# Performance work log

Measured on AMD Instinct MI355X. Metric: run time of the kernel, lower is better.

Reference implementation:

```python
import jax, jax.numpy as jnp
import numpy as np

B, S, H, L, NH, HD, V, FF, NC = 8, 512, 768, 12, 12, 64, 21128, 3072, 6
MAX_REL = 64
EPS = 1e-12


def rel_pos_table(seq_len, depth=HD, max_rel=MAX_REL):
    # NeZha functional (sinusoidal) relative-position embeddings, [S, S, depth]
    r = np.arange(seq_len)
    dist = np.clip(r[None, :] - r[:, None], -max_rel, max_rel) + max_rel
    vocab = 2 * max_rel + 1
    pos = np.arange(vocab)[:, None].astype(np.float32)
    i = np.arange(depth)[None, :]
    angle = pos / np.power(10000.0, (2 * (i // 2)) / float(depth))
    table = np.where(i % 2 == 0, np.sin(angle), np.cos(angle)).astype(np.float32)
    return jnp.asarray(table[dist])


def layer_norm(x, g, b):
    mu = jnp.mean(x, axis=-1, keepdims=True)
    var = jnp.mean(jnp.square(x - mu), axis=-1, keepdims=True)
    return (x - mu) * jax.lax.rsqrt(var + EPS) * g + b


def setup_inputs() -> dict:
    key = jax.random.key(0)
    ks = jax.random.split(key, 32)
    sd = 0.02
    d = {
        'input_ids': jax.random.randint(ks[0], (B, S), 0, V, dtype=jnp.int32),
        'attention_mask': jnp.ones((B, S), dtype=jnp.int32),
        'word_emb': sd * jax.random.normal(ks[1], (V, H), jnp.float32),
        'pos_emb': sd * jax.random.normal(ks[2], (S, H), jnp.float32),
        'type_emb': sd * jax.random.normal(ks[3], (2, H), jnp.float32),
        'ln_emb_g': jnp.ones((H,), jnp.float32),
        'ln_emb_b': jnp.zeros((H,), jnp.float32),
        'Wq': sd * jax.random.normal(ks[4], (L, H, H), jnp.float32),
        'bq': jnp.zeros((L, H), jnp.float32),
        'Wk': sd * jax.random.normal(ks[5], (L, H, H), jnp.float32),
        'bk': jnp.zeros((L, H), jnp.float32),
        'Wv': sd * jax.random.normal(ks[6], (L, H, H), jnp.float32),
        'bv': jnp.zeros((L, H), jnp.float32),
        'Wo': sd * jax.random.normal(ks[7], (L, H, H), jnp.float32),
        'bo': jnp.zeros((L, H), jnp.float32),
        'ln1_g': jnp.ones((L, H), jnp.float32),
        'ln1_b': jnp.zeros((L, H), jnp.float32),
        'W1': sd * jax.random.normal(ks[8], (L, H, FF), jnp.float32),
        'b1': jnp.zeros((L, FF), jnp.float32),
        'W2': sd * jax.random.normal(ks[9], (L, FF, H), jnp.float32),
        'b2': jnp.zeros((L, H), jnp.float32),
        'ln2_g': jnp.ones((L, H), jnp.float32),
        'ln2_b': jnp.zeros((L, H), jnp.float32),
        'pool_W': sd * jax.random.normal(ks[10], (H, H), jnp.float32),
        'pool_b': jnp.zeros((H,), jnp.float32),
        'cls_W': sd * jax.random.normal(ks[11], (2 * H, NC), jnp.float32),
        'cls_b': jnp.zeros((NC,), jnp.float32),
    }
    return d


def nezha_forward(input_ids, attention_mask, word_emb, pos_emb, type_emb,
                  ln_emb_g, ln_emb_b, Wq, bq, Wk, bk, Wv, bv, Wo, bo,
                  ln1_g, ln1_b, W1, b1, W2, b2, ln2_g, ln2_b,
                  pool_W, pool_b, cls_W, cls_b):
    seq = input_ids.shape[1]
    rel = rel_pos_table(seq)  # [S, S, HD], shared for keys and values
    mask_bias = (1.0 - attention_mask.astype(jnp.float32)) * -10000.0  # [B, S]

    x = word_emb[input_ids] + pos_emb[:seq][None, :, :] + type_emb[0][None, None, :]
    x = layer_norm(x, ln_emb_g, ln_emb_b)

    scale = 1.0 / jnp.sqrt(jnp.asarray(HD, jnp.float32))
    for l in range(L):
        q = (x @ Wq[l] + bq[l]).reshape(B, seq, NH, HD)
        k = (x @ Wk[l] + bk[l]).reshape(B, seq, NH, HD)
        v = (x @ Wv[l] + bv[l]).reshape(B, seq, NH, HD)
        # content scores + relative-position key scores
        scores = jnp.einsum('bihd,bjhd->bhij', q, k) + jnp.einsum('bihd,ijd->bhij', q, rel)
        scores = scores * scale + mask_bias[:, None, None, :]
        attn = jax.nn.softmax(scores, axis=-1)
        # content context + relative-position value context
        ctx = jnp.einsum('bhij,bjhd->bihd', attn, v) + jnp.einsum('bhij,ijd->bihd', attn, rel)
        ctx = ctx.reshape(B, seq, H)
        x = layer_norm(x + ctx @ Wo[l] + bo[l], ln1_g[l], ln1_b[l])
        h = jax.nn.gelu(x @ W1[l] + b1[l], approximate=False)
        x = layer_norm(x + h @ W2[l] + b2[l], ln2_g[l], ln2_b[l])

    pooled = jnp.tanh(x[:, 0] @ pool_W + pool_b)        # [B, H]
    seq_avg = jnp.mean(x, axis=1)                        # [B, H] (unmasked, as in torch.mean)
    concat = jnp.concatenate([seq_avg, pooled], axis=1)  # [B, 2H]
    return concat @ cls_W + cls_b                        # [B, 6]


def reference(input_ids, attention_mask, word_emb, pos_emb, type_emb,
              ln_emb_g, ln_emb_b, Wq, bq, Wk, bk, Wv, bv, Wo, bo,
              ln1_g, ln1_b, W1, b1, W2, b2, ln2_g, ln2_b,
              pool_W, pool_b, cls_W, cls_b):
    return nezha_forward(input_ids, attention_mask, word_emb, pos_emb, type_emb,
                         ln_emb_g, ln_emb_b, Wq, bq, Wk, bk, Wv, bv, Wo, bo,
                         ln1_g, ln1_b, W1, b1, W2, b2, ln2_g, ln2_b,
                         pool_W, pool_b, cls_W, cls_b)
```

## Files before the change

kernel.cpp:

```cpp
#include <hip/hip_runtime.h>
#include <hip/hip_bf16.h>
#include <math.h>

typedef __hip_bfloat16 bf;

#define B_ 8
#define S_ 512
#define H_ 768
#define L_ 12
#define NH_ 12
#define HD_ 64
#define FF_ 3072
#define NC_ 6
#define BS_ (B_ * S_)
#define BSH_ ((size_t)BS_ * H_)
#define KAUG_ 672
#define TAUG_ 160
#define TPAD_ 144

typedef __attribute__((ext_vector_type(8))) short s16x8;
typedef __attribute__((ext_vector_type(4))) float fx4;

__device__ __forceinline__ float LD(const void* p, size_t i, int isbf) {
    return isbf ? __bfloat162float(((const bf*)p)[i]) : ((const float*)p)[i];
}

__device__ __forceinline__ void gload16(const void* g, void* l) {
    __builtin_amdgcn_global_load_lds(
        (const __attribute__((address_space(1))) void*)g,
        (__attribute__((address_space(3))) void*)l, 16, 0, 0);
}

__device__ __forceinline__ s16x8 ldfrag64(const unsigned short* base, int row, int chunk) {
    return *(const s16x8*)((const char*)base + row * 128 + ((chunk ^ (row & 7)) << 4));
}
__device__ __forceinline__ s16x8 ldfrag32(const unsigned short* base, int row, int chunk) {
    return *(const s16x8*)((const char*)base + row * 64 + ((chunk ^ (row & 3)) << 4));
}

__device__ __forceinline__ float wred_sum(float v) {
#pragma unroll
    for (int o = 32; o; o >>= 1) v += __shfl_xor(v, o, 64);
    return v;
}
__device__ __forceinline__ float wred_max(float v) {
#pragma unroll
    for (int o = 32; o; o >>= 1) v = fmaxf(v, __shfl_xor(v, o, 64));
    return v;
}

__global__ void detect_kernel(const unsigned int* __restrict__ g, int* __restrict__ flag) {
    if (threadIdx.x == 0 && blockIdx.x == 0)
        *flag = (g[0] == 0x3F800000u) ? 0 : 1;
}

__global__ void build_table_kernel(float* __restrict__ tab) {
    int idx = blockIdx.x * 256 + threadIdx.x;
    if (idx >= 129 * 64) return;
    int p = idx >> 6, d = idx & 63;
    double angle = (double)p / pow(10000.0, (double)(2 * (d / 2)) / 64.0);
    tab[idx] = (float)((d & 1) ? cos(angle) : sin(angle));
}

__global__ void build_tabT_kernel(const float* __restrict__ tab,
                                  bf* __restrict__ th, bf* __restrict__ tl) {
    int idx = blockIdx.x * 256 + threadIdx.x;
    if (idx >= 64 * TAUG_) return;
    int d = idx / TAUG_, t = idx % TAUG_;
    float v = (t < 129) ? tab[t * 64 + d] : 0.0f;
    bf h = __float2bfloat16(v);
    th[idx] = h;
    tl[idx] = __float2bfloat16(v - __bfloat162float(h));
}

__global__ void build_tabS_kernel(const float* __restrict__ tab,
                                  bf* __restrict__ th, bf* __restrict__ tl) {
    int idx = blockIdx.x * 256 + threadIdx.x;
    if (idx >= TPAD_ * 64) return;
    int t = idx >> 6;
    float v = (t < 129) ? tab[idx] : 0.0f;
    bf h = __float2bfloat16(v);
    th[idx] = h;
    tl[idx] = __float2bfloat16(v - __bfloat162float(h));
}

__global__ __launch_bounds__(256) void embed_kernel(
    const int* __restrict__ ids, const void* __restrict__ we,
    const void* __restrict__ pe, const void* __restrict__ te,
    float* __restrict__ y, const int* __restrict__ fl) {
    int isbf = *fl;
    int t = blockIdx.x;
    int s = t & (S_ - 1);
    int id = ids[t];
    size_t base = (size_t)t * H_;
    for (int c = threadIdx.x; c < H_; c += 256) {
        y[base + c] = LD(we, (size_t)id * H_ + c, isbf) +
                      LD(pe, (size_t)s * H_ + c, isbf) +
                      LD(te, c, isbf);
    }
}

__global__ void maskbias_kernel(const int* __restrict__ mask, float* __restrict__ mb) {
    int t = blockIdx.x * 256 + threadIdx.x;
    if (t < BS_) mb[t] = (1.0f - (float)mask[t]) * -10000.0f;
}

__global__ __launch_bounds__(256) void ln_kernel(
    float* out, bf* ohi, bf* olo, const float* a, const float* resid,
    const void* __restrict__ g, const void* __restrict__ b, size_t goff,
    const int* __restrict__ fl) {
    __shared__ float part[256];
    int isbf = *fl;
    int tid = threadIdx.x;
    size_t base = (size_t)blockIdx.x * H_;
    float v0 = a[base + tid];
    float v1 = a[base + tid + 256];
    float v2 = a[base + tid + 512];
    if (resid) {
        v0 += resid[base + tid];
        v1 += resid[base + tid + 256];
        v2 += resid[base + tid + 512];
    }
    part[tid] = v0 + v1 + v2;
    __syncthreads();
    for (int off = 128; off > 0; off >>= 1) {
        if (tid < off) part[tid] += part[tid + off];
        __syncthreads();
    }
    float mu = part[0] * (1.0f / (float)H_);
    __syncthreads();
    float d0 = v0 - mu, d1 = v1 - mu, d2 = v2 - mu;
    part[tid] = d0 * d0 + d1 * d1 + d2 * d2;
    __syncthreads();
    for (int off = 128; off > 0; off >>= 1) {
        if (tid < off) part[tid] += part[tid + off];
        __syncthreads();
    }
    float var = part[0] * (1.0f / (float)H_);
    float rs = 1.0f / sqrtf(var + 1e-12f);
    float o0 = d0 * rs * LD(g, goff + tid, isbf)       + LD(b, goff + tid, isbf);
    float o1 = d1 * rs * LD(g, goff + tid + 256, isbf) + LD(b, goff + tid + 256, isbf);
    float o2 = d2 * rs * LD(g, goff + tid + 512, isbf) + LD(b, goff + tid + 512, isbf);
    out[base + tid]       = o0;
    out[base + tid + 256] = o1;
    out[base + tid + 512] = o2;
    if (ohi) {
        bf h0 = __float2bfloat16(o0), h1 = __float2bfloat16(o1), h2 = __float2bfloat16(o2);
        ohi[base + tid]       = h0;
        ohi[base + tid + 256] = h1;
        ohi[base + tid + 512] = h2;
        olo[base + tid]       = __float2bfloat16(o0 - __bfloat162float(h0));
        olo[base + tid + 256] = __float2bfloat16(o1 - __bfloat162float(h1));
        olo[base + tid + 512] = __float2bfloat16(o2 - __bfloat162float(h2));
    }
}

__global__ __launch_bounds__(256) void transpose_split_kernel(
    const void* __restrict__ W, size_t woff, bf* __restrict__ th, bf* __restrict__ tl,
    int K, int N, const int* __restrict__ fl) {
    __shared__ float s[32][33];
    const int isbf = *fl;
    const int tx = threadIdx.x & 31, ty = threadIdx.x >> 5;
    const int k0 = blockIdx.x * 32, n0 = blockIdx.y * 32;
#pragma unroll
    for (int i = 0; i < 4; ++i) {
        int k = k0 + ty + i * 8;
        s[ty + i * 8][tx] = LD(W, woff + (size_t)k * N + (n0 + tx), isbf);
    }
    __syncthreads();
#pragma unroll
    for (int i = 0; i < 4; ++i) {
        int n = n0 + ty + i * 8;
        float v = s[tx][ty + i * 8];
        bf h = __float2bfloat16(v);
        bf l = __float2bfloat16(v - __bfloat162float(h));
        th[(size_t)n * K + k0 + tx] = h;
        tl[(size_t)n * K + k0 + tx] = l;
    }
}

__global__ __launch_bounds__(256, 2) void mgemm_kernel(
    const bf* __restrict__ Ah, const bf* __restrict__ Al,
    const bf* __restrict__ Bh, const bf* __restrict__ Bl,
    const void* __restrict__ bias, size_t boff,
    float* __restrict__ C, bf* __restrict__ Chi, bf* __restrict__ Clo,
    int M, int N, int K, int act, int split_out, const int* __restrict__ fl) {
    (void)M;
    __shared__ __align__(16) unsigned short Ahs[128][32];
    __shared__ __align__(16) unsigned short Als[128][32];
    __shared__ __align__(16) unsigned short Bhs[128][32];
    __shared__ __align__(16) unsigned short Bls[128][32];
    const int tid  = threadIdx.x;
    const int lane = tid & 63;
    const int wid  = tid >> 6;
    const int wr   = wid >> 1, wc = wid & 1;
    const int m0 = blockIdx.y * 128, n0 = blockIdx.x * 128;
    const int srow = lane >> 2;
    const int scol = (lane & 3) * 8;

    const fx4 fzero = {0.f, 0.f, 0.f, 0.f};
    fx4 acc[4][4];
#pragma unroll
    for (int i = 0; i < 4; ++i)
#pragma unroll
        for (int j = 0; j < 4; ++j) acc[i][j] = fzero;

    for (int k0 = 0; k0 < K; k0 += 32) {
#pragma unroll
        for (int t = 0; t < 2; ++t) {
            const int r = wid * 32 + t * 16;
            const size_t ga = (size_t)(m0 + r + srow) * K + (k0 + scol);
            const size_t gb = (size_t)(n0 + r + srow) * K + (k0 + scol);
            gload16(Ah + ga, &Ahs[r][0]);
            gload16(Al + ga, &Als[r][0]);
            gload16(Bh + gb, &Bhs[r][0]);
            gload16(Bl + gb, &Bls[r][0]);
        }
        __syncthreads();

        const int fr = lane & 15;
        const int ko = (lane >> 4) * 8;
        s16x8 ah[4], al[4], bh[4], bl[4];
#pragma unroll
        for (int f = 0; f < 4; ++f) {
            ah[f] = *(const s16x8*)&Ahs[wr * 64 + f * 16 + fr][ko];
            al[f] = *(const s16x8*)&Als[wr * 64 + f * 16 + fr][ko];
            bh[f] = *(const s16x8*)&Bhs[wc * 64 + f * 16 + fr][ko];
            bl[f] = *(const s16x8*)&Bls[wc * 64 + f * 16 + fr][ko];
        }
#pragma unroll
        for (int im = 0; im < 4; ++im)
#pragma unroll
            for (int in = 0; in < 4; ++in) {
                acc[im][in] = __builtin_amdgcn_mfma_f32_16x16x32_bf16(ah[im], bh[in], acc[im][in], 0, 0, 0);
                acc[im][in] = __builtin_amdgcn_mfma_f32_16x16x32_bf16(ah[im], bl[in], acc[im][in], 0, 0, 0);
                acc[im][in] = __builtin_amdgcn_mfma_f32_16x16x32_bf16(al[im], bh[in], acc[im][in], 0, 0, 0);
            }
        __syncthreads();
    }

    const int isbf = *fl;
    const int cr0 = m0 + wr * 64 + (lane >> 4) * 4;
    const int cc0 = n0 + wc * 64 + (lane & 15);
#pragma unroll
    for (int in = 0; in < 4; ++in) {
        const int col = cc0 + in * 16;
        const float bv = LD(bias, boff + col, isbf);
#pragma unroll
        for (int im = 0; im < 4; ++im) {
#pragma unroll
            for (int r = 0; r < 4; ++r) {
                const int row = cr0 + im * 16 + r;
                float v = acc[im][in][r] + bv;
                if (act) v = 0.5f * v * (1.0f + erff(v * 0.70710678118654752f));
                if (split_out) {
                    bf h = __float2bfloat16(v);
                    bf l = __float2bfloat16(v - __bfloat162float(h));
                    Chi[(size_t)row * N + col] = h;
                    Clo[(size_t)row * N + col] = l;
                } else {
                    C[(size_t)row * N + col] = v;
                }
            }
        }
    }
}

__global__ __launch_bounds__(256) void qrel_kernel(
    const bf* __restrict__ qh, const bf* __restrict__ ql,
    const bf* __restrict__ tabSh, const bf* __restrict__ tabSl,
    float* __restrict__ qrel, int b0) {
    const int tid = threadIdx.x, lane = tid & 63, wv = tid >> 6;
    const int rbase = blockIdx.x * 128;
    const int h = blockIdx.y;
    const int t0 = blockIdx.z * 48;
    const int fr = lane & 15, ko = (lane >> 4) * 8;
    const fx4 fz = {0.f, 0.f, 0.f, 0.f};
    fx4 acc[2][3];
#pragma unroll
    for (int m = 0; m < 2; ++m)
#pragma unroll
        for (int n = 0; n < 3; ++n) acc[m][n] = fz;
#pragma unroll
    for (int ks = 0; ks < 2; ++ks) {
        s16x8 a_h[2], a_l[2], b_h[3], b_l[3];
#pragma unroll
        for (int m = 0; m < 2; ++m) {
            const int row = rbase + wv * 32 + m * 16 + fr;
            const size_t ga = ((size_t)(b0 * S_) + row) * H_ + h * 64 + ks * 32 + ko;
            a_h[m] = *(const s16x8*)(qh + ga);
            a_l[m] = *(const s16x8*)(ql + ga);
        }
#pragma unroll
        for (int n = 0; n < 3; ++n) {
            const int trow = t0 + n * 16 + fr;
            const size_t gb = (size_t)trow * 64 + ks * 32 + ko;
            b_h[n] = *(const s16x8*)(tabSh + gb);
            b_l[n] = *(const s16x8*)(tabSl + gb);
        }
#pragma unroll
        for (int m = 0; m < 2; ++m)
#pragma unroll
            for (int n = 0; n < 3; ++n) {
                acc[m][n] = __builtin_amdgcn_mfma_f32_16x16x32_bf16(a_h[m], b_h[n], acc[m][n], 0, 0, 0);
                acc[m][n] = __builtin_amdgcn_mfma_f32_16x16x32_bf16(a_h[m], b_l[n], acc[m][n], 0, 0, 0);
                acc[m][n] = __builtin_amdgcn_mfma_f32_16x16x32_bf16(a_l[m], b_h[n], acc[m][n], 0, 0, 0);
            }
    }
    const int rr = (lane >> 4) * 4, cc = lane & 15;
#pragma unroll
    for (int m = 0; m < 2; ++m)
#pragma unroll
        for (int n = 0; n < 3; ++n)
#pragma unroll
            for (int r = 0; r < 3 + 1; ++r) {
                const int row = rbase + wv * 32 + m * 16 + rr + r;
                const int t = t0 + n * 16 + cc;
                const int bb = row >> 9, ii = row & (S_ - 1);
                qrel[(((size_t)bb * NH_ + h) * S_ + ii) * TPAD_ + t] = acc[m][n][r];
            }
}

__global__ __launch_bounds__(256, 2) void qk_kernel(
    const bf* __restrict__ qh, const bf* __restrict__ ql,
    const bf* __restrict__ kh, const bf* __restrict__ kl,
    float* __restrict__ sc, int b0) {
    __shared__ __align__(16) unsigned short Qh[128][64];
    __shared__ __align__(16) unsigned short Ql_[128][64];
    __shared__ __align__(16) unsigned short Kh[128][64];
    __shared__ __align__(16) unsigned short Kl[128][64];
    const int tid = threadIdx.x, lane = tid & 63, wv = tid >> 6;
    const int j0 = blockIdx.x * 128, i0 = blockIdx.y * 128;
    const int h = blockIdx.z % NH_, bb = blockIdx.z / NH_;
    const int b = b0 + bb;
    const int srow = lane >> 3;
    const int schunk = (lane & 7) ^ (srow & 7);
#pragma unroll
    for (int t = 0; t < 4; ++t) {
        const int r = wv * 32 + t * 8;
        const size_t ga = (size_t)(b * S_ + i0 + r + srow) * H_ + h * 64 + schunk * 8;
        const size_t gb = (size_t)(b * S_ + j0 + r + srow) * H_ + h * 64 + schunk * 8;
        gload16(qh + ga, &Qh[r][0]);
        gload16(ql + ga, &Ql_[r][0]);
        gload16(kh + gb, &Kh[r][0]);
        gload16(kl + gb, &Kl[r][0]);
    }
    __syncthreads();
    const int fr = lane & 15, g = lane >> 4;
    const int wr = wv >> 1, wc = wv & 1;
    const fx4 fz = {0.f, 0.f, 0.f, 0.f};
    fx4 acc[4][4];
#pragma unroll
    for (int i = 0; i < 4; ++i)
#pragma unroll
        for (int j = 0; j < 4; ++j) acc[i][j] = fz;
#pragma unroll
    for (int ks = 0; ks < 2; ++ks) {
        s16x8 ah[4], al[4], bh[4], bl[4];
#pragma unroll
        for (int m = 0; m < 4; ++m) {
            const int row = wr * 64 + m * 16 + fr;
            ah[m] = ldfrag64(&Qh[0][0], row, ks * 4 + g);
            al[m] = ldfrag64(&Ql_[0][0], row, ks * 4 + g);
        }
#pragma unroll
        for (int n = 0; n < 4; ++n) {
            const int row = wc * 64 + n * 16 + fr;
            bh[n] = ldfrag64(&Kh[0][0], row, ks * 4 + g);
            bl[n] = ldfrag64(&Kl[0][0], row, ks * 4 + g);
        }
#pragma unroll
        for (int m = 0; m < 4; ++m)
#pragma unroll
            for (int n = 0; n < 4; ++n) {
                acc[m][n] = __builtin_amdgcn_mfma_f32_16x16x32_bf16(ah[m], bh[n], acc[m][n], 0, 0, 0);
                acc[m][n] = __builtin_amdgcn_mfma_f32_16x16x32_bf16(ah[m], bl[n], acc[m][n], 0, 0, 0);
                acc[m][n] = __builtin_amdgcn_mfma_f32_16x16x32_bf16(al[m], bh[n], acc[m][n], 0, 0, 0);
            }
    }
    const int rr = (lane >> 4) * 4, cc = lane & 15;
#pragma unroll
    for (int m = 0; m < 4; ++m)
#pragma unroll
        for (int n = 0; n < 4; ++n)
#pragma unroll
            for (int r = 0; r < 4; ++r) {
                const int ii = i0 + wr * 64 + m * 16 + rr + r;
                const int jj = j0 + wc * 64 + n * 16 + cc;
                sc[(((size_t)bb * NH_ + h) * S_ + ii) * S_ + jj] = acc[m][n][r];
            }
}

__global__ __launch_bounds__(256) void smrel_kernel(
    const float* __restrict__ scores, const float* __restrict__ qrel,
    const float* __restrict__ mb,
    bf* __restrict__ pah, bf* __restrict__ pal, int b0) {
    const int lane = threadIdx.x & 63;
    const int wv = threadIdx.x >> 6;
    const int i = blockIdx.x * 4 + wv;
    const int h = blockIdx.y, bb = blockIdx.z;
    const int b = b0 + bb;
    const size_t srow = ((size_t)bb * NH_ + h) * S_ + i;
    const size_t qbase = srow * TPAD_;
    const float mbias = mb[b * S_ + lane] * 0.0f + 0.0f; (void)mbias;

    float s[8];
    float lmax = -1e30f;
#pragma unroll
    for (int rep = 0; rep < 8; ++rep) {
        const int j = lane + rep * 64;
        int t = j - i; t = t < -64 ? -64 : (t > 64 ? 64 : t);
        float v = (scores[srow * S_ + j] + qrel[qbase + t + 64]) * 0.125f + mb[b * S_ + j];
        s[rep] = v;
        lmax = fmaxf(lmax, v);
    }
    const float mx = wred_max(lmax);
    float lsum = 0.0f;
#pragma unroll
    for (int rep = 0; rep < 8; ++rep) {
        s[rep] = expf(s[rep] - mx);
        lsum += s[rep];
    }
    const float inv = 1.0f / wred_sum(lsum);

    const size_t rowbase = srow * KAUG_;
#pragma unroll
    for (int e = 0; e < 3; ++e) {
        const int t = lane + e * 64;
        if (t < TAUG_) {
            pah[rowbase + 512 + t] = __float2bfloat16(0.0f);
            pal[rowbase + 512 + t] = __float2bfloat16(0.0f);
        }
    }
    float s_lo = 0.0f, s_hi = 0.0f;
#pragma unroll
    for (int rep = 0; rep < 8; ++rep) {
        const int j = lane + rep * 64;
        const float v = s[rep] * inv;
        bf hh = __float2bfloat16(v);
        pah[rowbase + j] = hh;
        pal[rowbase + j] = __float2bfloat16(v - __bfloat162float(hh));
        const int d = j - i;
        if (d <= -64) s_lo += s[rep];
        else if (d >= 64) s_hi += s[rep];
        else {
            pah[rowbase + 512 + d + 64] = hh;
            pal[rowbase + 512 + d + 64] = __float2bfloat16(v - __bfloat162float(hh));
        }
    }
    s_lo = wred_sum(s_lo);
    s_hi = wred_sum(s_hi);
    if (lane == 0) {
        float v0 = s_lo * inv;
        bf h0 = __float2bfloat16(v0);
        pah[rowbase + 512] = h0;
        pal[rowbase + 512] = __float2bfloat16(v0 - __bfloat162float(h0));
        float v1 = s_hi * inv;
        bf h1 = __float2bfloat16(v1);
        pah[rowbase + 512 + 128] = h1;
        pal[rowbase + 512 + 128] = __float2bfloat16(v1 - __bfloat162float(h1));
    }
}

__global__ __launch_bounds__(256) void vaug_kernel(
    const bf* __restrict__ vh, const bf* __restrict__ vl,
    const bf* __restrict__ tabTh, const bf* __restrict__ tabTl,
    bf* __restrict__ vah, bf* __restrict__ val_, int b0) {
    __shared__ unsigned short tile[64][71];
    const int h = blockIdx.x, pl = blockIdx.y, bb = blockIdx.z;
    const int b = b0 + bb;
    const bf* src  = pl ? vl : vh;
    bf*       dst  = pl ? val_ : vah;
    const bf* tsrc = pl ? tabTl : tabTh;
    const int tid = threadIdx.x;
    const size_t dbase = ((size_t)bb * NH_ + h) * 64;
    for (int j0 = 0; j0 < S_; j0 += 64) {
        for (int idx = tid; idx < 4096; idx += 256) {
            int jj = idx >> 6, d = idx & 63;
            tile[jj][d] = *(const unsigned short*)&src[(size_t)(b * S_ + j0 + jj) * H_ + h * 64 + d];
        }
        __syncthreads();
        for (int idx = tid; idx < 4096; idx += 256) {
            int d = idx >> 6, jj = idx & 63;
            *(unsigned short*)&dst[(dbase + d) * KAUG_ + j0 + jj] = tile[jj][d];
        }
        __syncthreads();
    }
    for (int idx = tid; idx < 64 * TAUG_; idx += 256) {
        int d = idx / TAUG_, t = idx % TAUG_;
        *(unsigned short*)&dst[(dbase + d) * KAUG_ + 512 + t] =
            *(const unsigned short*)&tsrc[idx];
    }
}

__global__ __launch_bounds__(256, 2) void pv_kernel(
    const bf* __restrict__ pah, const bf* __restrict__ pal,
    const bf* __restrict__ vah, const bf* __restrict__ val_,
    bf* __restrict__ ch, bf* __restrict__ cl, int b0) {
    __shared__ __align__(16) unsigned short Ah[128][32];
    __shared__ __align__(16) unsigned short Al[128][32];
    __shared__ __align__(16) unsigned short Bh[64][32];
    __shared__ __align__(16) unsigned short Bl[64][32];
    const int tid = threadIdx.x, lane = tid & 63, wv = tid >> 6;
    const int h = blockIdx.x, i0 = blockIdx.y * 128, bb = blockIdx.z;
    const int b = b0 + bb;
    const int srow = lane >> 2;
    const int schunk = (lane & 3) ^ (srow & 3);
    const fx4 fz = {0.f, 0.f, 0.f, 0.f};
    fx4 acc[2][4];
#pragma unroll
    for (int m = 0; m < 2; ++m)
#pragma unroll
        for (int n = 0; n < 4; ++n) acc[m][n] = fz;

    for (int k0 = 0; k0 < KAUG_; k0 += 32) {
#pragma unroll
        for (int t = 0; t < 2; ++t) {
            const int r = wv * 32 + t * 16;
            const size_t ga = (((size_t)bb * NH_ + h) * S_ + i0 + r + srow) * KAUG_ + k0 + schunk * 8;
            gload16(pah + ga, &Ah[r][0]);
            gload16(pal + ga, &Al[r][0]);
        }
        {
            const int r = wv * 16;
            const size_t gb = (((size_t)bb * NH_ + h) * 64 + r + srow) * KAUG_ + k0 + schunk * 8;
            gload16(vah + gb, &Bh[r][0]);
            gload16(val_ + gb, &Bl[r][0]);
        }
        __syncthreads();
        const int fr = lane & 15, g = lane >> 4;
        s16x8 a_h[2], a_l[2], b_h[4], b_l[4];
#pragma unroll
        for (int m = 0; m < 2; ++m) {
            const int row = wv * 32 + m * 16 + fr;
            a_h[m] = ldfrag32(&Ah[0][0], row, g);
            a_l[m] = ldfrag32(&Al[0][0], row, g);
        }
#pragma unroll
        for (int n = 0; n < 4; ++n) {
            const int row = n * 16 + fr;
            b_h[n] = ldfrag32(&Bh[0][0], row, g);
            b_l[n] = ldfrag32(&Bl[0][0], row, g);
        }
#pragma unroll
        for (int m = 0; m < 2; ++m)
#pragma unroll
            for (int n = 0; n < 4; ++n) {
                acc[m][n] = __builtin_amdgcn_mfma_f32_16x16x32_bf16(a_h[m], b_h[n], acc[m][n], 0, 0, 0);
                acc[m][n] = __builtin_amdgcn_mfma_f32_16x16x32_bf16(a_h[m], b_l[n], acc[m][n], 0, 0, 0);
                acc[m][n] = __builtin_amdgcn_mfma_f32_16x16x32_bf16(a_l[m], b_h[n], acc[m][n], 0, 0, 0);
            }
        __syncthreads();
    }
    const int rr = (lane >> 4) * 4, cc = lane & 15;
#pragma unroll
    for (int m = 0; m < 2; ++m)
#pragma unroll
        for (int n = 0; n < 4; ++n)
#pragma unroll
            for (int r = 0; r < 4; ++r) {
                const int row = i0 + wv * 32 + m * 16 + rr + r;
                const int d = n * 16 + cc;
                const float v = acc[m][n][r];
                bf hh = __float2bfloat16(v);
                const size_t o = (size_t)(b * S_ + row) * H_ + h * 64 + d;
                ch[o] = hh;
                cl[o] = __float2bfloat16(v - __bfloat162float(hh));
            }
}

__global__ __launch_bounds__(256) void pool_kernel(
    const float* __restrict__ x, const void* __restrict__ pW,
    const void* __restrict__ pb, float* __restrict__ pooled,
    const int* __restrict__ fl) {
    int isbf = *fl;
    int b = blockIdx.x;
    const float* xr = x + (size_t)b * S_ * H_;
    for (int n = threadIdx.x; n < H_; n += 256) {
        float acc = LD(pb, n, isbf);
        for (int kx = 0; kx < H_; ++kx)
            acc += xr[kx] * LD(pW, (size_t)kx * H_ + n, isbf);
        pooled[b * H_ + n] = tanhf(acc);
    }
}

__global__ __launch_bounds__(256) void seqavg_kernel(
    const float* __restrict__ x, float* __restrict__ sa) {
    int b = blockIdx.x;
    for (int c = threadIdx.x; c < H_; c += 256) {
        float s = 0.0f;
        for (int j = 0; j < S_; ++j) s += x[((size_t)b * S_ + j) * H_ + c];
        sa[b * H_ + c] = s * (1.0f / (float)S_);
    }
}

__global__ void head_kernel(const float* __restrict__ sa, const float* __restrict__ pooled,
                            const void* __restrict__ cW, const void* __restrict__ cb,
                            void* __restrict__ out, const int* __restrict__ fl) {
    int isbf = *fl;
    int t = threadIdx.x;
    if (t >= B_ * NC_) return;
    int b = t / NC_, c = t % NC_;
    float acc = LD(cb, c, isbf);
    for (int kx = 0; kx < H_; ++kx)
        acc += sa[b * H_ + kx] * LD(cW, (size_t)kx * NC_ + c, isbf);
    for (int kx = 0; kx < H_; ++kx)
        acc += pooled[b * H_ + kx] * LD(cW, (size_t)(H_ + kx) * NC_ + c, isbf);
    if (isbf) ((bf*)out)[t] = __float2bfloat16(acc);
    else      ((float*)out)[t] = acc;
}

extern "C" void kernel_launch(void* const* d_in, const int* in_sizes, int n_in,
                              void* d_out, int out_size, void* d_ws, size_t ws_size,
                              hipStream_t stream) {
    (void)in_sizes; (void)n_in; (void)out_size;
    const int* ids   = (const int*)d_in[0];
    const int* amask = (const int*)d_in[1];
    const void* we  = d_in[2];
    const void* pe  = d_in[3];
    const void* te  = d_in[4];
    const void* lng = d_in[5];
    const void* lnb = d_in[6];
    const void* Wq  = d_in[7];
    const void* bq  = d_in[8];
    const void* Wk  = d_in[9];
    const void* bk  = d_in[10];
    const void* Wv  = d_in[11];
    const void* bv  = d_in[12];
    const void* Wo  = d_in[13];
    const void* bo  = d_in[14];
    const void* l1g = d_in[15];
    const void* l1b = d_in[16];
    const void* W1  = d_in[17];
    const void* b1  = d_in[18];
    const void* W2  = d_in[19];
    const void* b2  = d_in[20];
    const void* l2g = d_in[21];
    const void* l2b = d_in[22];
    const void* pW  = d_in[23];
    const void* pb  = d_in[24];
    const void* cW  = d_in[25];
    const void* cb  = d_in[26];

    char* cur = (char*)d_ws;
    auto alloc = [&](size_t bytes) -> char* {
        char* p = cur;
        cur += (bytes + 255) & ~(size_t)255;
        return p;
    };
    float* x    = (float*)alloc(BSH_ * 4);
    float* r0   = (float*)alloc(BSH_ * 4);
    float* r1f  = (float*)alloc(BSH_ * 4);
    float* r2f  = (float*)alloc(BSH_ * 4);
    float* r3f  = (float*)alloc(BSH_ * 4);
    float* z    = (float*)alloc(BSH_ * 4);
    float* tab  = (float*)alloc(129 * 64 * 4);
    float* mb   = (float*)alloc(BS_ * 4);
    float* pool = (float*)alloc(B_ * H_ * 4);
    float* sa   = (float*)alloc(B_ * H_ * 4);
    bf* tabTh   = (bf*)alloc(64 * TAUG_ * 2);
    bf* tabTl   = (bf*)alloc(64 * TAUG_ * 2);
    bf* tabSh   = (bf*)alloc(TPAD_ * 64 * 2);
    bf* tabSl   = (bf*)alloc(TPAD_ * 64 * 2);
    int* flag   = (int*)alloc(256);

    const size_t fixed = (size_t)(cur - (char*)d_ws);
    auto regA_sz = [&](int CB) {
        size_t wt = (size_t)2 * H_ * FF_ * 2;
        size_t qr = (size_t)CB * NH_ * S_ * TPAD_ * 4;
        return (wt > qr ? wt : qr);
    };
    auto regB_sz = [&](int CB) {
        size_t xs = (size_t)4 * BSH_;
        size_t sc = (size_t)CB * NH_ * S_ * S_ * 4;
        return (xs > sc ? xs : sc);
    };
    auto need = [&](int CB) {
        return fixed + regA_sz(CB) + regB_sz(CB)
             + (size_t)CB * NH_ * S_ * KAUG_ * 2 * 2
             + (size_t)CB * NH_ * 64 * KAUG_ * 2 * 2
             + 4096;
    };
    int CB = 8;
    while (CB > 1 && need(CB) > ws_size) CB >>= 1;

    char* regA = alloc(regA_sz(CB));
    char* regB = alloc(regB_sz(CB));
    bf* pah  = (bf*)alloc((size_t)CB * NH_ * S_ * KAUG_ * 2 * 2);
    bf* pal  = pah + (size_t)CB * NH_ * S_ * KAUG_;
    bf* vah  = (bf*)alloc((size_t)CB * NH_ * 64 * KAUG_ * 2 * 2);
    bf* val_ = vah + (size_t)CB * NH_ * 64 * KAUG_;

    bf*    wth   = (bf*)regA;
    bf*    wtl   = wth + (size_t)H_ * FF_;
    float* qrelb = (float*)regA;
    bf*    xh    = (bf*)regB;
    bf*    xl    = xh + BSH_;
    float* scb   = (float*)regB;

    bf* qh  = (bf*)r1f; bf* qlp = qh  + BSH_;
    bf* khp = (bf*)r2f; bf* klp = khp + BSH_;
    bf* vhp = (bf*)r3f; bf* vlp = vhp + BSH_;
    bf* ch  = (bf*)r0;  bf* cl  = ch  + BSH_;
    bf* hbh = (bf*)r0;
    bf* hbl = (bf*)r2f;

    detect_kernel<<<1, 64, 0, stream>>>((const unsigned int*)lng, flag);
    build_table_kernel<<<(129 * 64 + 255) / 256, 256, 0, stream>>>(tab);
    build_tabT_kernel<<<(64 * TAUG_ + 255) / 256, 256, 0, stream>>>(tab, tabTh, tabTl);
    build_tabS_kernel<<<(TPAD_ * 64 + 255) / 256, 256, 0, stream>>>(tab, tabSh, tabSl);
    maskbias_kernel<<<(BS_ + 255) / 256, 256, 0, stream>>>(amask, mb);
    embed_kernel<<<BS_, 256, 0, stream>>>(ids, we, pe, te, r0, flag);
    ln_kernel<<<BS_, 256, 0, stream>>>(x, xh, xl, r0, nullptr, lng, lnb, 0, flag);

    dim3 tpHH(H_ / 32, H_ / 32);
    dim3 tpHF(H_ / 32, FF_ / 32);
    dim3 tpFH(FF_ / 32, H_ / 32);
    dim3 gH(H_ / 128, BS_ / 128);
    dim3 gF(FF_ / 128, BS_ / 128);
    dim3 gQR(CB * S_ / 128, NH_, 3);
    dim3 gVA(NH_, 2, CB);
    dim3 gQK(4, 4, NH_ * CB);
    dim3 gSM(S_ / 4, NH_, CB);
    dim3 gPV(NH_, 4, CB);

    for (int l = 0; l < L_; ++l) {
        const size_t oHH = (size_t)l * H_ * H_;
        const size_t oH  = (size_t)l * H_;
        const size_t oHF = (size_t)l * H_ * FF_;
        const size_t oF  = (size_t)l * FF_;

        transpose_split_kernel<<<tpHH, 256, 0, stream>>>(Wq, oHH, wth, wtl, H_, H_, flag);
        mgemm_kernel<<<gH, 256, 0, stream>>>(xh, xl, wth, wtl, bq, oH,
                                             nullptr, qh, qlp, BS_, H_, H_, 0, 1, flag);
        transpose_split_kernel<<<tpHH, 256, 0, stream>>>(Wk, oHH, wth, wtl, H_, H_, flag);
        mgemm_kernel<<<gH, 256, 0, stream>>>(xh, xl, wth, wtl, bk, oH,
                                             nullptr, khp, klp, BS_, H_, H_, 0, 1, flag);
        transpose_split_kernel<<<tpHH, 256, 0, stream>>>(Wv, oHH, wth, wtl, H_, H_, flag);
        mgemm_kernel<<<gH, 256, 0, stream>>>(xh, xl, wth, wtl, bv, oH,
                                             nullptr, vhp, vlp, BS_, H_, H_, 0, 1, flag);

        for (int b0 = 0; b0 < B_; b0 += CB) {
            qrel_kernel<<<gQR, 256, 0, stream>>>(qh, qlp, tabSh, tabSl, qrelb, b0);
            vaug_kernel<<<gVA, 256, 0, stream>>>(vhp, vlp, tabTh, tabTl, vah, val_, b0);
            qk_kernel<<<gQK, 256, 0, stream>>>(qh, qlp, khp, klp, scb, b0);
            smrel_kernel<<<gSM, 256, 0, stream>>>(scb, qrelb, mb, pah, pal, b0);
            pv_kernel<<<gPV, 256, 0, stream>>>(pah, pal, vah, val_, ch, cl, b0);
        }

        transpose_split_kernel<<<tpHH, 256, 0, stream>>>(Wo, oHH, wth, wtl, H_, H_, flag);
        mgemm_kernel<<<gH, 256, 0, stream>>>(ch, cl, wth, wtl, bo, oH,
                                             r1f, nullptr, nullptr, BS_, H_, H_, 0, 0, flag);
        ln_kernel<<<BS_, 256, 0, stream>>>(x, xh, xl, r1f, x, l1g, l1b, oH, flag);

        transpose_split_kernel<<<tpHF, 256, 0, stream>>>(W1, oHF, wth, wtl, H_, FF_, flag);
        mgemm_kernel<<<gF, 256, 0, stream>>>(xh, xl, wth, wtl, b1, oF,
                                             nullptr, hbh, hbl, BS_, FF_, H_, 1, 1, flag);
        transpose_split_kernel<<<tpFH, 256, 0, stream>>>(W2, oHF, wth, wtl, FF_, H_, flag);
        mgemm_kernel<<<gH, 256, 0, stream>>>(hbh, hbl, wth, wtl, b2, oH,
                                             z, nullptr, nullptr, BS_, H_, FF_, 0, 0, flag);
        ln_kernel<<<BS_, 256, 0, stream>>>(x, xh, xl, z, x, l2g, l2b, oH, flag);
    }

    pool_kernel<<<B_, 256, 0, stream>>>(x, pW, pb, pool, flag);
    seqavg_kernel<<<B_, 256, 0, stream>>>(x, sa);
    head_kernel<<<1, 64, 0, stream>>>(sa, pool, cW, cb, d_out, flag);
}
```

Baseline: 7.814 ms.

## Fuse QKV projections into one GEMM, add 64-row GEMM tiles, warp-per-row layernorm

Transposes Wq/Wk/Wv into one concatenated weight buffer, precomputes a concatenated fp32 bias, and runs a single GEMM with row stride 2304 so attention kernels read Q/K/V through a stride argument. The GEMM is templated on row tiles, and the H-output GEMMs use 64-row tiles to double block count for the small-N cases. Layernorm now uses one wavefront per row with shuffle reductions instead of a 256-thread block with shared-memory tree reductions. These aim to cut launch count, improve occupancy on narrow GEMMs, and remove barrier-heavy reductions, at the cost of a larger QKV buffer and workspace layout changes.

```diff
diff --git a/kernel.cpp b/kernel.cpp
--- a/kernel.cpp
+++ b/kernel.cpp
@@ -17,6 +17,7 @@
 #define KAUG_ 672
 #define TAUG_ 160
 #define TPAD_ 144
+#define QSTR_ 2304
 
 typedef __attribute__((ext_vector_type(8))) short s16x8;
 typedef __attribute__((ext_vector_type(4))) float fx4;
@@ -50,8 +51,10 @@
 }
 
 __global__ void detect_kernel(const unsigned int* __restrict__ g, int* __restrict__ flag) {
-    if (threadIdx.x == 0 && blockIdx.x == 0)
-        *flag = (g[0] == 0x3F800000u) ? 0 : 1;
+    if (threadIdx.x == 0 && blockIdx.x == 0) {
+        flag[0] = (g[0] == 0x3F800000u) ? 0 : 1;
+        flag[1] = 0;
+    }
 }
 
 __global__ void build_table_kernel(float* __restrict__ tab) {
@@ -105,53 +108,49 @@
     if (t < BS_) mb[t] = (1.0f - (float)mask[t]) * -10000.0f;
 }
 
+__global__ void biascat_kernel(const void* __restrict__ bq, const void* __restrict__ bk,
+                               const void* __restrict__ bv, size_t off,
+                               float* __restrict__ out, const int* __restrict__ fl) {
+    int isbf = *fl;
+    int t = blockIdx.x * 256 + threadIdx.x;
+    if (t >= 3 * H_) return;
+    const void* src = t < H_ ? bq : (t < 2 * H_ ? bk : bv);
+    out[t] = LD(src, off + (t % H_), isbf);
+}
+
 __global__ __launch_bounds__(256) void ln_kernel(
     float* out, bf* ohi, bf* olo, const float* a, const float* resid,
     const void* __restrict__ g, const void* __restrict__ b, size_t goff,
     const int* __restrict__ fl) {
-    __shared__ float part[256];
-    int isbf = *fl;
-    int tid = threadIdx.x;
-    size_t base = (size_t)blockIdx.x * H_;
-    float v0 = a[base + tid];
-    float v1 = a[base + tid + 256];
-    float v2 = a[base + tid + 512];
-    if (resid) {
-        v0 += resid[base + tid];
-        v1 += resid[base + tid + 256];
-        v2 += resid[base + tid + 512];
-    }
-    part[tid] = v0 + v1 + v2;
-    __syncthreads();
-    for (int off = 128; off > 0; off >>= 1) {
-        if (tid < off) part[tid] += part[tid + off];
-        __syncthreads();
-    }
-    float mu = part[0] * (1.0f / (float)H_);
-    __syncthreads();
-    float d0 = v0 - mu, d1 = v1 - mu, d2 = v2 - mu;
-    part[tid] = d0 * d0 + d1 * d1 + d2 * d2;
-    __syncthreads();
-    for (int off = 128; off > 0; off >>= 1) {
-        if (tid < off) part[tid] += part[tid + off];
-        __syncthreads();
-    }
-    float var = part[0] * (1.0f / (float)H_);
-    float rs = 1.0f / sqrtf(var + 1e-12f);
-    float o0 = d0 * rs * LD(g, goff + tid, isbf)       + LD(b, goff + tid, isbf);
-    float o1 = d1 * rs * LD(g, goff + tid + 256, isbf) + LD(b, goff + tid + 256, isbf);
-    float o2 = d2 * rs * LD(g, goff + tid + 512, isbf) + LD(b, goff + tid + 512, isbf);
-    out[base + tid]       = o0;
-    out[base + tid + 256] = o1;
-    out[base + tid + 512] = o2;
-    if (ohi) {
-        bf h0 = __float2bfloat16(o0), h1 = __float2bfloat16(o1), h2 = __float2bfloat16(o2);
-        ohi[base + tid]       = h0;
-        ohi[base + tid + 256] = h1;
-        ohi[base + tid + 512] = h2;
-        olo[base + tid]       = __float2bfloat16(o0 - __bfloat162float(h0));
-        olo[base + tid + 256] = __float2bfloat16(o1 - __bfloat162float(h1));
-        olo[base + tid + 512] = __float2bfloat16(o2 - __bfloat162float(h2));
+    const int isbf = *fl;
+    const int lane = threadIdx.x & 63, wv = threadIdx.x >> 6;
+    const int row = blockIdx.x * 4 + wv;
+    const size_t base = (size_t)row * H_;
+    float v[12];
+#pragma unroll
+    for (int e = 0; e < 12; ++e) {
+        const int c = lane + e * 64;
+        v[e] = a[base + c];
+        if (resid) v[e] += resid[base + c];
+    }
+    float s = 0.0f;
+#pragma unroll
+    for (int e = 0; e < 12; ++e) s += v[e];
+    const float mu = wred_sum(s) * (1.0f / (float)H_);
+    float q = 0.0f;
+#pragma unroll
+    for (int e = 0; e < 12; ++e) { v[e] -= mu; q += v[e] * v[e]; }
+    const float rs = 1.0f / sqrtf(wred_sum(q) * (1.0f / (float)H_) + 1e-12f);
+#pragma unroll
+    for (int e = 0; e < 12; ++e) {
+        const int c = lane + e * 64;
+        float o = v[e] * rs * LD(g, goff + c, isbf) + LD(b, goff + c, isbf);
+        out[base + c] = o;
+        if (ohi) {
+            bf h = __float2bfloat16(o);
+            ohi[base + c] = h;
+            olo[base + c] = __float2bfloat16(o - __bfloat162float(h));
+        }
     }
 }
 
@@ -179,40 +178,44 @@
     }
 }
 
+template<int MR>
 __global__ __launch_bounds__(256, 2) void mgemm_kernel(
     const bf* __restrict__ Ah, const bf* __restrict__ Al,
     const bf* __restrict__ Bh, const bf* __restrict__ Bl,
     const void* __restrict__ bias, size_t boff,
     float* __restrict__ C, bf* __restrict__ Chi, bf* __restrict__ Clo,
-    int M, int N, int K, int act, int split_out, const int* __restrict__ fl) {
-    (void)M;
-    __shared__ __align__(16) unsigned short Ahs[128][32];
-    __shared__ __align__(16) unsigned short Als[128][32];
+    int N, int K, int act, int split_out, const int* __restrict__ fl) {
+    __shared__ __align__(16) unsigned short Ahs[MR * 32][32];
+    __shared__ __align__(16) unsigned short Als[MR * 32][32];
     __shared__ __align__(16) unsigned short Bhs[128][32];
     __shared__ __align__(16) unsigned short Bls[128][32];
     const int tid  = threadIdx.x;
     const int lane = tid & 63;
     const int wid  = tid >> 6;
     const int wr   = wid >> 1, wc = wid & 1;
-    const int m0 = blockIdx.y * 128, n0 = blockIdx.x * 128;
+    const int m0 = blockIdx.y * (MR * 32), n0 = blockIdx.x * 128;
     const int srow = lane >> 2;
     const int scol = (lane & 3) * 8;
 
     const fx4 fzero = {0.f, 0.f, 0.f, 0.f};
-    fx4 acc[4][4];
-#pragma unroll
-    for (int i = 0; i < 4; ++i)
+    fx4 acc[MR][4];
+#pragma unroll
+    for (int i = 0; i < MR; ++i)
 #pragma unroll
         for (int j = 0; j < 4; ++j) acc[i][j] = fzero;
 
     for (int k0 = 0; k0 < K; k0 += 32) {
+#pragma unroll
+        for (int t = 0; t < MR / 2; ++t) {
+            const int r = wid * (MR * 8) + t * 16;
+            const size_t ga = (size_t)(m0 + r + srow) * K + (k0 + scol);
+            gload16(Ah + ga, &Ahs[r][0]);
+            gload16(Al + ga, &Als[r][0]);
+        }
 #pragma unroll
         for (int t = 0; t < 2; ++t) {
             const int r = wid * 32 + t * 16;
-            const size_t ga = (size_t)(m0 + r + srow) * K + (k0 + scol);
             const size_t gb = (size_t)(n0 + r + srow) * K + (k0 + scol);
-            gload16(Ah + ga, &Ahs[r][0]);
-            gload16(Al + ga, &Als[r][0]);
             gload16(Bh + gb, &Bhs[r][0]);
             gload16(Bl + gb, &Bls[r][0]);
         }
@@ -220,16 +223,19 @@
 
         const int fr = lane & 15;
         const int ko = (lane >> 4) * 8;
-        s16x8 ah[4], al[4], bh[4], bl[4];
+        s16x8 ah[MR], al[MR], bh[4], bl[4];
+#pragma unroll
+        for (int f = 0; f < MR; ++f) {
+            ah[f] = *(const s16x8*)&Ahs[wr * (MR * 16) + f * 16 + fr][ko];
+            al[f] = *(const s16x8*)&Als[wr * (MR * 16) + f * 16 + fr][ko];
+        }
 #pragma unroll
         for (int f = 0; f < 4; ++f) {
-            ah[f] = *(const s16x8*)&Ahs[wr * 64 + f * 16 + fr][ko];
-            al[f] = *(const s16x8*)&Als[wr * 64 + f * 16 + fr][ko];
             bh[f] = *(const s16x8*)&Bhs[wc * 64 + f * 16 + fr][ko];
             bl[f] = *(const s16x8*)&Bls[wc * 64 + f * 16 + fr][ko];
         }
 #pragma unroll
-        for (int im = 0; im < 4; ++im)
+        for (int im = 0; im < MR; ++im)
 #pragma unroll
             for (int in = 0; in < 4; ++in) {
                 acc[im][in] = __builtin_amdgcn_mfma_f32_16x16x32_bf16(ah[im], bh[in], acc[im][in], 0, 0, 0);
@@ -240,14 +246,14 @@
     }
 
     const int isbf = *fl;
-    const int cr0 = m0 + wr * 64 + (lane >> 4) * 4;
+    const int cr0 = m0 + wr * (MR * 16) + (lane >> 4) * 4;
     const int cc0 = n0 + wc * 64 + (lane & 15);
 #pragma unroll
     for (int in = 0; in < 4; ++in) {
         const int col = cc0 + in * 16;
         const float bv = LD(bias, boff + col, isbf);
 #pragma unroll
-        for (int im = 0; im < 4; ++im) {
+        for (int im = 0; im < MR; ++im) {
 #pragma unroll
             for (int r = 0; r < 4; ++r) {
                 const int row = cr0 + im * 16 + r;
@@ -269,7 +275,7 @@
 __global__ __launch_bounds__(256) void qrel_kernel(
     const bf* __restrict__ qh, const bf* __restrict__ ql,
     const bf* __restrict__ tabSh, const bf* __restrict__ tabSl,
-    float* __restrict__ qrel, int b0) {
+    float* __restrict__ qrel, int astr, int b0) {
     const int tid = threadIdx.x, lane = tid & 63, wv = tid >> 6;
     const int rbase = blockIdx.x * 128;
     const int h = blockIdx.y;
@@ -287,7 +293,7 @@
 #pragma unroll
         for (int m = 0; m < 2; ++m) {
             const int row = rbase + wv * 32 + m * 16 + fr;
-            const size_t ga = ((size_t)(b0 * S_) + row) * H_ + h * 64 + ks * 32 + ko;
+            const size_t ga = ((size_t)(b0 * S_) + row) * astr + h * 64 + ks * 32 + ko;
             a_h[m] = *(const s16x8*)(qh + ga);
             a_l[m] = *(const s16x8*)(ql + ga);
         }
@@ -313,7 +319,7 @@
 #pragma unroll
         for (int n = 0; n < 3; ++n)
 #pragma unroll
-            for (int r = 0; r < 3 + 1; ++r) {
+            for (int r = 0; r < 4; ++r) {
                 const int row = rbase + wv * 32 + m * 16 + rr + r;
                 const int t = t0 + n * 16 + cc;
                 const int bb = row >> 9, ii = row & (S_ - 1);
@@ -324,7 +330,7 @@
 __global__ __launch_bounds__(256, 2) void qk_kernel(
     const bf* __restrict__ qh, const bf* __restrict__ ql,
     const bf* __restrict__ kh, const bf* __restrict__ kl,
-    float* __restrict__ sc, int b0) {
+    float* __restrict__ sc, int astr, int b0) {
     __shared__ __align__(16) unsigned short Qh[128][64];
     __shared__ __align__(16) unsigned short Ql_[128][64];
     __shared__ __align__(16) unsigned short Kh[128][64];
@@ -338,8 +344,8 @@
 #pragma unroll
     for (int t = 0; t < 4; ++t) {
         const int r = wv * 32 + t * 8;
-        const size_t ga = (size_t)(b * S_ + i0 + r + srow) * H_ + h * 64 + schunk * 8;
-        const size_t gb = (size_t)(b * S_ + j0 + r + srow) * H_ + h * 64 + schunk * 8;
+        const size_t ga = (size_t)(b * S_ + i0 + r + srow) * astr + h * 64 + schunk * 8;
+        const size_t gb = (size_t)(b * S_ + j0 + r + srow) * astr + h * 64 + schunk * 8;
         gload16(qh + ga, &Qh[r][0]);
         gload16(ql + ga, &Ql_[r][0]);
         gload16(kh + gb, &Kh[r][0]);
@@ -402,7 +408,6 @@
     const int b = b0 + bb;
     const size_t srow = ((size_t)bb * NH_ + h) * S_ + i;
     const size_t qbase = srow * TPAD_;
-    const float mbias = mb[b * S_ + lane] * 0.0f + 0.0f; (void)mbias;
 
     float s[8];
     float lmax = -1e30f;
@@ -465,7 +470,7 @@
 __global__ __launch_bounds__(256) void vaug_kernel(
     const bf* __restrict__ vh, const bf* __restrict__ vl,
     const bf* __restrict__ tabTh, const bf* __restrict__ tabTl,
-    bf* __restrict__ vah, bf* __restrict__ val_, int b0) {
+    bf* __restrict__ vah, bf* __restrict__ val_, int astr, int b0) {
     __shared__ unsigned short tile[64][71];
     const int h = blockIdx.x, pl = blockIdx.y, bb = blockIdx.z;
     const int b = b0 + bb;
@@ -477,7 +482,7 @@
     for (int j0 = 0; j0 < S_; j0 += 64) {
         for (int idx = tid; idx < 4096; idx += 256) {
             int jj = idx >> 6, d = idx & 63;
-            tile[jj][d] = *(const unsigned short*)&src[(size_t)(b * S_ + j0 + jj) * H_ + h * 64 + d];
+            tile[jj][d] = *(const unsigned short*)&src[(size_t)(b * S_ + j0 + jj) * astr + h * 64 + d];
         }
         __syncthreads();
         for (int idx = tid; idx < 4096; idx += 256) {
@@ -658,11 +663,13 @@
     float* mb   = (float*)alloc(BS_ * 4);
     float* pool = (float*)alloc(B_ * H_ * 4);
     float* sa   = (float*)alloc(B_ * H_ * 4);
+    float* bqkv = (float*)alloc(3 * H_ * 4);
     bf* tabTh   = (bf*)alloc(64 * TAUG_ * 2);
     bf* tabTl   = (bf*)alloc(64 * TAUG_ * 2);
     bf* tabSh   = (bf*)alloc(TPAD_ * 64 * 2);
     bf* tabSl   = (bf*)alloc(TPAD_ * 64 * 2);
     int* flag   = (int*)alloc(256);
+    int* zflag  = flag + 1;
 
     const size_t fixed = (size_t)(cur - (char*)d_ws);
     auto regA_sz = [&](int CB) {
@@ -698,12 +705,11 @@
     bf*    xl    = xh + BSH_;
     float* scb   = (float*)regB;
 
-    bf* qh  = (bf*)r1f; bf* qlp = qh  + BSH_;
-    bf* khp = (bf*)r2f; bf* klp = khp + BSH_;
-    bf* vhp = (bf*)r3f; bf* vlp = vhp + BSH_;
-    bf* ch  = (bf*)r0;  bf* cl  = ch  + BSH_;
-    bf* hbh = (bf*)r0;
-    bf* hbl = (bf*)r2f;
+    bf* qkvh = (bf*)r1f;
+    bf* qkvl = qkvh + (size_t)BS_ * QSTR_;
+    bf* ch   = (bf*)r0;  bf* cl = ch + BSH_;
+    bf* hbh  = (bf*)r0;
+    bf* hbl  = (bf*)r2f;
 
     detect_kernel<<<1, 64, 0, stream>>>((const unsigned int*)lng, flag);
     build_table_kernel<<<(129 * 64 + 255) / 256, 256, 0, stream>>>(tab);
@@ -711,12 +717,13 @@
     build_tabS_kernel<<<(TPAD_ * 64 + 255) / 256, 256, 0, stream>>>(tab, tabSh, tabSl);
     maskbias_kernel<<<(BS_ + 255) / 256, 256, 0, stream>>>(amask, mb);
     embed_kernel<<<BS_, 256, 0, stream>>>(ids, we, pe, te, r0, flag);
-    ln_kernel<<<BS_, 256, 0, stream>>>(x, xh, xl, r0, nullptr, lng, lnb, 0, flag);
+    ln_kernel<<<BS_ / 4, 256, 0, stream>>>(x, xh, xl, r0, nullptr, lng, lnb, 0, flag);
 
     dim3 tpHH(H_ / 32, H_ / 32);
     dim3 tpHF(H_ / 32, FF_ / 32);
     dim3 tpFH(FF_ / 32, H_ / 32);
-    dim3 gH(H_ / 128, BS_ / 128);
+    dim3 gQKV(3 * H_ / 128, BS_ / 128);
+    dim3 gH64(H_ / 128, BS_ / 64);
     dim3 gF(FF_ / 128, BS_ / 128);
     dim3 gQR(CB * S_ / 128, NH_, 3);
     dim3 gVA(NH_, 2, CB);
@@ -731,35 +738,36 @@
         const size_t oF  = (size_t)l * FF_;
 
         transpose_split_kernel<<<tpHH, 256, 0, stream>>>(Wq, oHH, wth, wtl, H_, H_, flag);
-        mgemm_kernel<<<gH, 256, 0, stream>>>(xh, xl, wth, wtl, bq, oH,
-                                             nullptr, qh, qlp, BS_, H_, H_, 0, 1, flag);
-        transpose_split_kernel<<<tpHH, 256, 0, stream>>>(Wk, oHH, wth, wtl, H_, H_, flag);
-        mgemm_kernel<<<gH, 256, 0, stream>>>(xh, xl, wth, wtl, bk, oH,
-                                             nullptr, khp, klp, BS_, H_, H_, 0, 1, flag);
-        transpose_split_kernel<<<tpHH, 256, 0, stream>>>(Wv, oHH, wth, wtl, H_, H_, flag);
-        mgemm_kernel<<<gH, 256, 0, stream>>>(xh, xl, wth, wtl, bv, oH,
-                                             nullptr, vhp, vlp, BS_, H_, H_, 0, 1, flag);
+        transpose_split_kernel<<<tpHH, 256, 0, stream>>>(Wk, oHH,
+            wth + (size_t)H_ * H_, wtl + (size_t)H_ * H_, H_, H_, flag);
+        transpose_split_kernel<<<tpHH, 256, 0, stream>>>(Wv, oHH,
+            wth + (size_t)2 * H_ * H_, wtl + (size_t)2 * H_ * H_, H_, H_, flag);
+        biascat_kernel<<<(3 * H_ + 255) / 256, 256, 0, stream>>>(bq, bk, bv, oH, bqkv, flag);
+        mgemm_kernel<4><<<gQKV, 256, 0, stream>>>(xh, xl, wth, wtl, bqkv, 0,
+            nullptr, qkvh, qkvl, QSTR_, H_, 0, 1, zflag);
 
         for (int b0 = 0; b0 < B_; b0 += CB) {
-            qrel_kernel<<<gQR, 256, 0, stream>>>(qh, qlp, tabSh, tabSl, qrelb, b0);
-            vaug_kernel<<<gVA, 256, 0, stream>>>(vhp, vlp, tabTh, tabTl, vah, val_, b0);
-            qk_kernel<<<gQK, 256, 0, stream>>>(qh, qlp, khp, klp, scb, b0);
+            qrel_kernel<<<gQR, 256, 0, stream>>>(qkvh, qkvl, tabSh, tabSl, qrelb, QSTR_, b0);
+            vaug_kernel<<<gVA, 256, 0, stream>>>(qkvh + 2 * H_, qkvl + 2 * H_,
+                tabTh, tabTl, vah, val_, QSTR_, b0);
+            qk_kernel<<<gQK, 256, 0, stream>>>(qkvh, qkvl, qkvh + H_, qkvl + H_,
+                scb, QSTR_, b0);
             smrel_kernel<<<gSM, 256, 0, stream>>>(scb, qrelb, mb, pah, pal, b0);
             pv_kernel<<<gPV, 256, 0, stream>>>(pah, pal, vah, val_, ch, cl, b0);
         }
 
         transpose_split_kernel<<<tpHH, 256, 0, stream>>>(Wo, oHH, wth, wtl, H_, H_, flag);
-        mgemm_kernel<<<gH, 256, 0, stream>>>(ch, cl, wth, wtl, bo, oH,
-                                             r1f, nullptr, nullptr, BS_, H_, H_, 0, 0, flag);
-        ln_kernel<<<BS_, 256, 0, stream>>>(x, xh, xl, r1f, x, l1g, l1b, oH, flag);
+        mgemm_kernel<2><<<gH64, 256, 0, stream>>>(ch, cl, wth, wtl, bo, oH,
+            z, nullptr, nullptr, H_, H_, 0, 0, flag);
+        ln_kernel<<<BS_ / 4, 256, 0, stream>>>(x, xh, xl, z, x, l1g, l1b, oH, flag);
 
         transpose_split_kernel<<<tpHF, 256, 0, stream>>>(W1, oHF, wth, wtl, H_, FF_, flag);
-        mgemm_kernel<<<gF, 256, 0, stream>>>(xh, xl, wth, wtl, b1, oF,
-                                             nullptr, hbh, hbl, BS_, FF_, H_, 1, 1, flag);
+        mgemm_kernel<4><<<gF, 256, 0, stream>>>(xh, xl, wth, wtl, b1, oF,
+            nullptr, hbh, hbl, FF_, H_, 1, 1, flag);
         transpose_split_kernel<<<tpFH, 256, 0, stream>>>(W2, oHF, wth, wtl, FF_, H_, flag);
-        mgemm_kernel<<<gH, 256, 0, stream>>>(hbh, hbl, wth, wtl, b2, oH,
-                                             z, nullptr, nullptr, BS_, H_, FF_, 0, 0, flag);
-        ln_kernel<<<BS_, 256, 0, stream>>>(x, xh, xl, z, x, l2g, l2b, oH, flag);
+        mgemm_kernel<2><<<gH64, 256, 0, stream>>>(hbh, hbl, wth, wtl, b2, oH,
+            z, nullptr, nullptr, H_, FF_, 0, 0, flag);
+        ln_kernel<<<BS_ / 4, 256, 0, stream>>>(x, xh, xl, z, x, l2g, l2b, oH, flag);
     }
 
     pool_kernel<<<B_, 256, 0, stream>>>(x, pW, pb, pool, flag);
```

Measured after the change: 6.869 ms. -12.1%, faster.
